# Kernel tuning notes

Measured on AMD Instinct MI355X. Metric: run time of the kernel, lower is better.

The kernel has to match this reference:

```python
import jax, jax.numpy as jnp
import numpy as np
from jax.scipy.special import gammaln, betaln

B, S, F, D, FEAT = 8, 128, 512, 256, 80


def conv1d(x, w, b, pad):
    # x: (B, C_in, L), w: (C_out, C_in, K) -> (B, C_out, L)
    y = jax.lax.conv_general_dilated(x, w, window_strides=(1,), padding=[(pad, pad)],
                                     dimension_numbers=('NCH', 'OIH', 'NCH'))
    return y + b[None, :, None]


def beta_binomial_log_prior(token_length, feat_length):
    # Vectorized betabinom(n=L-1, a=j+1, b=F_len-j).logpmf(k) over (B, S, F).
    k = jnp.arange(S, dtype=jnp.float32)[None, :, None]
    j = jnp.arange(F, dtype=jnp.float32)[None, None, :]
    L = token_length.astype(jnp.float32)[:, None, None]
    Fl = feat_length.astype(jnp.float32)[:, None, None]
    valid = (k < L) & (j < Fl)
    n = jnp.maximum(L - 1.0, 0.0)
    ks = jnp.minimum(k, n)                 # clamp outside-support k (masked anyway)
    a = j + 1.0                            # omega=1: a = i, i = j+1
    b = jnp.maximum(Fl - j, 1.0)           # b = F_len - i + 1 = F_len - j
    log_binom = gammaln(n + 1.0) - gammaln(ks + 1.0) - gammaln(n - ks + 1.0)
    lp = log_binom + betaln(ks + a, n - ks + b) - betaln(a, b)
    return jnp.where(valid, lp, -jnp.inf)


def setup_inputs() -> dict:
    key = jax.random.key(0)
    ks = jax.random.split(key, 10)
    h = jax.random.normal(ks[0], (B, S, D), jnp.float32)
    m = jax.random.normal(ks[1], (B, F, FEAT), jnp.float32)
    token_length = jax.random.randint(ks[2], (B,), S // 2, S + 1, dtype=jnp.int32)
    feat_length = jax.random.randint(ks[3], (B,), F // 2, F + 1, dtype=jnp.int32)
    mask = jnp.arange(S)[None, :] < token_length[:, None]
    w = lambda k, sh: jax.random.normal(k, sh, jnp.float32) * 0.02
    return dict(
        h=h, m=m,
        tw1=w(ks[4], (D, D, 3)), tb1=jnp.zeros((D,), jnp.float32),
        tw2=w(ks[5], (D, D, 1)), tb2=jnp.zeros((D,), jnp.float32),
        fw1=w(ks[6], (D, FEAT, 3)), fb1=jnp.zeros((D,), jnp.float32),
        fw2=w(ks[7], (D, D, 3)), fb2=jnp.zeros((D,), jnp.float32),
        fw3=w(ks[8], (D, D, 1)), fb3=jnp.zeros((D,), jnp.float32),
        mask=mask, token_length=token_length, feat_length=feat_length,
    )


def reference(h, m, tw1, tb1, tw2, tb2, fw1, fb1, fw2, fb2, fw3, fb3,
              mask, token_length, feat_length):
    # text conv stack: conv3(relu) -> conv1
    x = conv1d(h.transpose(0, 2, 1), tw1, tb1, 1)
    x = conv1d(jax.nn.relu(x), tw2, tb2, 0)
    hh = x.transpose(0, 2, 1)              # (B, S, D)
    # feat conv stack: conv3(relu) -> conv3(relu) -> conv1
    y = conv1d(m.transpose(0, 2, 1), fw1, fb1, 1)
    y = conv1d(jax.nn.relu(y), fw2, fb2, 1)
    y = conv1d(jax.nn.relu(y), fw3, fb3, 0)
    mm = y.transpose(0, 2, 1)              # (B, F, D)
    # broadcasted L2 pairwise distance -> (B, S, F)
    diff = hh[:, :, None, :] - mm[:, None, :, :]
    dist = jnp.sqrt(jnp.sum(diff * diff, axis=-1))
    logit = jnp.where(mask[:, :, None], -dist, -jnp.inf)
    log_a_soft = jax.nn.log_softmax(logit, axis=1)
    log_prior = beta_binomial_log_prior(token_length, feat_length)
    return log_prior + log_a_soft
```

## Files before the change

### kernel.cpp

```cpp
#include <hip/hip_runtime.h>
#include <cmath>

constexpr int B = 8, S = 128, F = 512, D = 256, FEAT = 80;
#define NEG_HUGE (-3.0e38f)

typedef unsigned short u16;
typedef unsigned int u32;
typedef __attribute__((ext_vector_type(8))) short bf16x8;
typedef __attribute__((ext_vector_type(4))) float f32x4;

#define MFMA(a, b, c) __builtin_amdgcn_mfma_f32_16x16x32_bf16((a), (b), (c), 0, 0, 0)

__device__ __forceinline__ u16 f2bf(float x) {
    u32 u = __float_as_uint(x);
    return (u16)((u + 0x7fffu + ((u >> 16) & 1u)) >> 16);
}
__device__ __forceinline__ float bf2f(u16 s) {
    return __uint_as_float(((u32)s) << 16);
}

constexpr int PRF = F + 2;
constexpr int PRH = S + 2;
constexpr int CIN_M = 96;

constexpr int N_G   = 1024;
constexpr int N_WT1 = 256 * 768;
constexpr int N_WT2 = 256 * 256;
constexpr int N_WF1 = 256 * 288;
constexpr int N_WF2 = 256 * 768;
constexpr int N_WF3 = 256 * 256;
constexpr int N_M   = B * PRF * CIN_M;
constexpr int N_H   = B * PRH * D;
constexpr int N_Y1P = B * 2 * D;
constexpr int PREP_TOTAL = N_G + N_WT1 + N_WT2 + N_WF1 + N_WF2 + N_WF3
                         + N_M + N_H + N_Y1P;

__device__ __forceinline__ void wconv_frag(const float* __restrict__ w,
                                           u16* __restrict__ o16,
                                           int I, int TAPS, int CINP, int idx) {
    int KSTEPS = TAPS * CINP / 32;
    int e    = idx & 7;
    int lane = (idx >> 3) & 63;
    int rest = idx >> 9;
    int kb   = rest % KSTEPS;
    int ct16 = rest / KSTEPS;
    int co = ct16 * 16 + (lane & 15);
    int k  = kb * 32 + (lane >> 4) * 8 + e;
    int tap = k / CINP, ci = k % CINP;
    float v = (ci < I) ? w[(co * I + ci) * TAPS + tap] : 0.f;
    o16[idx] = f2bf(v);
}

__global__ __launch_bounds__(256) void k_prep(
    const float* __restrict__ m, const float* __restrict__ h,
    const float* __restrict__ tw1, const float* __restrict__ tw2,
    const float* __restrict__ fw1, const float* __restrict__ fw2,
    const float* __restrict__ fw3,
    float* __restrict__ gt,
    u16* __restrict__ WT1, u16* __restrict__ WT2,
    u16* __restrict__ WF1, u16* __restrict__ WF2, u16* __restrict__ WF3,
    u16* __restrict__ M, u16* __restrict__ H, u16* __restrict__ Y1)
{
    int idx = blockIdx.x * 256 + threadIdx.x;
    if (idx < N_G) { gt[idx] = (float)lgamma((double)idx); return; }
    idx -= N_G;
    if (idx < N_WT1) { wconv_frag(tw1, WT1, 256, 3, 256, idx); return; }
    idx -= N_WT1;
    if (idx < N_WT2) { wconv_frag(tw2, WT2, 256, 1, 256, idx); return; }
    idx -= N_WT2;
    if (idx < N_WF1) { wconv_frag(fw1, WF1,  80, 3, CIN_M, idx); return; }
    idx -= N_WF1;
    if (idx < N_WF2) { wconv_frag(fw2, WF2, 256, 3, 256, idx); return; }
    idx -= N_WF2;
    if (idx < N_WF3) { wconv_frag(fw3, WF3, 256, 1, 256, idx); return; }
    idx -= N_WF3;
    if (idx < N_M) {
        int ci = idx % CIN_M;
        int p  = (idx / CIN_M) % PRF;
        int b  = idx / (CIN_M * PRF);
        float v = (p >= 1 && p <= F && ci < FEAT)
                ? m[(b * F + (p - 1)) * FEAT + ci] : 0.f;
        M[idx] = f2bf(v);
        return;
    }
    idx -= N_M;
    if (idx < N_H) {
        int ci = idx % D;
        int p  = (idx / D) % PRH;
        int b  = idx / (D * PRH);
        float v = (p >= 1 && p <= S) ? h[(b * S + (p - 1)) * D + ci] : 0.f;
        H[idx] = f2bf(v);
        return;
    }
    idx -= N_H;
    if (idx < N_Y1P) {
        int ci = idx % D;
        int which = (idx / D) & 1;
        int b = idx / (2 * D);
        int row = b * PRF + (which ? (PRF - 1) : 0);
        Y1[row * D + ci] = 0;
    }
}

constexpr int SHBYTES = 17408;

template<int CINP, int TAPS, bool RELU>
__device__ __forceinline__ void conv_block(
    char* shbuf,
    const u16* __restrict__ A, int arowbase,
    const u16* __restrict__ Wf, const float* __restrict__ bias, int co0,
    u16* __restrict__ O, int orowbase)
{
    constexpr int KTOT = TAPS * CINP;
    constexpr int KSTEPS = KTOT / 32;
    constexpr int KPT = CINP / 32;
    constexpr int ITER = (KSTEPS + 3) / 4;
    constexpr int ROWS = 32 + TAPS - 1;
    constexpr int RB = CINP * 2;

    const int t  = threadIdx.x;
    const int w  = t >> 6;
    const int l  = t & 63;
    const int lr = l & 15;
    const int kg = l >> 4;

    for (int c = t; c < ROWS * (CINP / 8); c += 256) {
        int row = c / (CINP / 8), cc = c % (CINP / 8);
        bf16x8 v = *(const bf16x8*)(A + (arowbase + row) * CINP + cc * 8);
        *(bf16x8*)(shbuf + row * RB + ((cc * 16) ^ ((row & 7) << 4))) = v;
    }
    __syncthreads();

    f32x4 a00 = {0.f, 0.f, 0.f, 0.f}, a01 = a00, a10 = a00, a11 = a00;
    const u16* wp0 = Wf + (size_t)(co0 >> 4) * KSTEPS * 512 + l * 8;
    const u16* wp1 = wp0 + (size_t)KSTEPS * 512;

#pragma unroll
    for (int i = 0; i < ITER; ++i) {
        int kb = w + 4 * i;
        if (KSTEPS % 4 == 0 || kb < KSTEPS) {
            int colb = (kb % KPT) * 64 + kg * 16;
            int rr0 = lr + kb / KPT;
            int rr1 = rr0 + 16;
            bf16x8 ah0 = *(const bf16x8*)(shbuf + rr0 * RB + (colb ^ ((rr0 & 7) << 4)));
            bf16x8 ah1 = *(const bf16x8*)(shbuf + rr1 * RB + (colb ^ ((rr1 & 7) << 4)));
            bf16x8 b0  = *(const bf16x8*)(wp0 + kb * 512);
            bf16x8 b1  = *(const bf16x8*)(wp1 + kb * 512);
            a00 = MFMA(ah0, b0, a00);
            a01 = MFMA(ah0, b1, a01);
            a10 = MFMA(ah1, b0, a10);
            a11 = MFMA(ah1, b1, a11);
        }
    }
    __syncthreads();

    float (*red)[64][17] = (float(*)[64][17])shbuf;
#pragma unroll
    for (int r = 0; r < 4; ++r) {
        red[w][l][0 * 4 + r] = a00[r];
        red[w][l][1 * 4 + r] = a01[r];
        red[w][l][2 * 4 + r] = a10[r];
        red[w][l][3 * 4 + r] = a11[r];
    }
    __syncthreads();

#pragma unroll
    for (int j = 0; j < 4; ++j) {
        int v = w * 4 + j;
        float s = red[0][l][v] + red[1][l][v] + red[2][l][v] + red[3][l][v];
        int m2 = v >> 3, ct = (v >> 2) & 1, r = v & 3;
        int co = co0 + ct * 16 + lr;
        int orow = orowbase + m2 * 16 + kg * 4 + r;
        float val = s + bias[co];
        if (RELU) val = fmaxf(val, 0.f);
        O[orow * 256 + co] = f2bf(val);
    }
}

__global__ __launch_bounds__(256) void k_convA(
    const u16* __restrict__ M, const u16* __restrict__ H,
    const u16* __restrict__ WF1, const u16* __restrict__ WT1,
    const float* __restrict__ fb1, const float* __restrict__ tb1,
    u16* __restrict__ Y1, u16* __restrict__ X1)
{
    __shared__ __align__(16) char shbuf[SHBYTES];
    int bid = blockIdx.x;
    if (bid < 1024) {
        int co0 = (bid & 7) * 32;
        int p0  = ((bid >> 3) & 15) * 32;
        int b   = bid >> 7;
        conv_block<CIN_M, 3, true>(shbuf, M, b * PRF + p0, WF1, fb1, co0,
                                   Y1, b * PRF + p0 + 1);
    } else {
        int i = bid - 1024;
        int co0 = (i & 7) * 32;
        int p0  = ((i >> 3) & 3) * 32;
        int b   = i >> 5;
        conv_block<D, 3, true>(shbuf, H, b * PRH + p0, WT1, tb1, co0,
                               X1, b * S + p0);
    }
}

__global__ __launch_bounds__(256) void k_convB(
    const u16* __restrict__ Y1, const u16* __restrict__ X1,
    const u16* __restrict__ WF2, const u16* __restrict__ WT2,
    const float* __restrict__ fb2, const float* __restrict__ tb2,
    u16* __restrict__ Y2, u16* __restrict__ Ho)
{
    __shared__ __align__(16) char shbuf[SHBYTES];
    int bid = blockIdx.x;
    if (bid < 1024) {
        int co0 = (bid & 7) * 32;
        int p0  = ((bid >> 3) & 15) * 32;
        int b   = bid >> 7;
        conv_block<D, 3, true>(shbuf, Y1, b * PRF + p0, WF2, fb2, co0,
                               Y2, b * F + p0);
    } else {
        int i = bid - 1024;
        int co0 = (i & 7) * 32;
        int p0  = ((i >> 3) & 3) * 32;
        int b   = i >> 5;
        conv_block<D, 1, false>(shbuf, X1, b * S + p0, WT2, tb2, co0,
                                Ho, b * S + p0);
    }
}

__global__ __launch_bounds__(512) void k_distsoft(
    const u16* __restrict__ Y2, const u16* __restrict__ Ho,
    const u16* __restrict__ WF3, const float* __restrict__ fb3,
    const float* __restrict__ gt,
    const int* __restrict__ tokl, const int* __restrict__ featl,
    float* __restrict__ out)
{
    __shared__ float gts[1024];
    __shared__ u16 mo[16 * 256];
    __shared__ float sc[128][18];
    __shared__ float red[512];
    __shared__ float na[128], nb[16], mcol[16], scol[16];
    int t = threadIdx.x;
    int b = blockIdx.x >> 5;
    int f0 = (blockIdx.x & 31) * 16;
    for (int i = t; i < 1024; i += 512) gts[i] = gt[i];
    int L = tokl[b], Fl = featl[b];

    int w = t >> 6, l = t & 63, lr = l & 15, kg = (l >> 4) & 3;

    {
        f32x4 acc0 = {0.f, 0.f, 0.f, 0.f}, acc1 = acc0;
        const u16* ap = Y2 + (b * F + f0 + lr) * 256 + kg * 8;
        const u16* wp = WF3 + (size_t)(2 * w) * 8 * 512 + l * 8;
#pragma unroll
        for (int kb = 0; kb < 8; ++kb) {
            bf16x8 av = *(const bf16x8*)(ap + kb * 32);
            bf16x8 b0 = *(const bf16x8*)(wp + kb * 512);
            bf16x8 b1 = *(const bf16x8*)(wp + (8 + kb) * 512);
            acc0 = MFMA(av, b0, acc0);
            acc1 = MFMA(av, b1, acc1);
        }
#pragma unroll
        for (int nt = 0; nt < 2; ++nt) {
            int co = w * 32 + nt * 16 + lr;
            float bv = fb3[co];
            const f32x4& a = nt == 0 ? acc0 : acc1;
#pragma unroll
            for (int r = 0; r < 4; ++r) {
                int pos = kg * 4 + r;
                int byte = pos * 512 + ((co * 2) ^ ((pos & 7) << 4));
                *(u16*)((char*)mo + byte) = f2bf(a[r] + bv);
            }
        }
    }
    __syncthreads();

    {
        int c = t >> 5;
        int byte = c * 512 + (((t & 31) * 16) ^ ((c & 7) << 4));
        bf16x8 v = *(const bf16x8*)((char*)mo + byte);
        float s = 0.f;
#pragma unroll
        for (int e = 0; e < 8; ++e) { float a = bf2f((u16)v[e]); s = fmaf(a, a, s); }
        red[t] = s;
    }
    __syncthreads();
    if (t < 16) {
        float s = 0.f;
#pragma unroll
        for (int j = 0; j < 32; ++j) s += red[t * 32 + j];
        nb[t] = s;
    }
    __syncthreads();

    {
        int r = t >> 2, kc = (t & 3) * 64;
        const u16* p = Ho + (b * S + r) * 256 + kc;
        float s = 0.f;
#pragma unroll
        for (int j = 0; j < 8; ++j) {
            bf16x8 v = *(const bf16x8*)(p + j * 8);
#pragma unroll
            for (int e = 0; e < 8; ++e) { float a = bf2f((u16)v[e]); s = fmaf(a, a, s); }
        }
        red[t] = s;
    }
    __syncthreads();
    if (t < 128) na[t] = red[4 * t] + red[4 * t + 1] + red[4 * t + 2] + red[4 * t + 3];

    f32x4 acc = {0.f, 0.f, 0.f, 0.f};
    {
        const u16* ap = Ho + (b * S + w * 16 + lr) * 256 + kg * 8;
        const char* bbase = (const char*)mo + lr * 512;
        int bx = (lr & 7) << 4;
#pragma unroll
        for (int kb = 0; kb < 8; ++kb) {
            bf16x8 a0 = *(const bf16x8*)(ap + kb * 32);
            bf16x8 bv = *(const bf16x8*)(bbase + ((kg * 16 + kb * 64) ^ bx));
            acc = MFMA(a0, bv, acc);
        }
    }
    __syncthreads();
#pragma unroll
    for (int r = 0; r < 4; ++r) {
        int sl = w * 16 + kg * 4 + r;
        float d2 = na[sl] + nb[lr] - 2.f * acc[r];
        sc[sl][lr] = -sqrtf(fmaxf(d2, 0.f));
    }
    __syncthreads();

    int fi = t & 15, sg = t >> 4;
    float sv[4], mx = -INFINITY;
#pragma unroll
    for (int i = 0; i < 4; ++i) {
        int s = sg + i * 32;
        float v = sc[s][fi];
        if (s >= L) v = -INFINITY;
        sv[i] = v;
        mx = fmaxf(mx, v);
    }
    red[t] = mx;
    __syncthreads();
    if (t < 16) {
        float m2 = -INFINITY;
#pragma unroll
        for (int j = 0; j < 32; ++j) m2 = fmaxf(m2, red[j * 16 + t]);
        mcol[t] = m2;
    }
    __syncthreads();
    float m = mcol[fi];
    float sum = 0.f;
#pragma unroll
    for (int i = 0; i < 4; ++i) sum += expf(sv[i] - m);
    red[t] = sum;
    __syncthreads();
    if (t < 16) {
        float s = 0.f;
#pragma unroll
        for (int j = 0; j < 32; ++j) s += red[j * 16 + t];
        scol[t] = s;
    }
    __syncthreads();
    float lse = m + logf(scol[fi]);

    int f = f0 + fi;
    float cb = gts[L] - gts[L + Fl] + gts[Fl + 1];
    bool fvalid = f < Fl;
    float cf = fvalid ? (-gts[f + 1] - gts[Fl - f]) : 0.f;
#pragma unroll
    for (int i = 0; i < 4; ++i) {
        int s = sg + i * 32;
        float o;
        if (s >= L || !fvalid) {
            o = NEG_HUGE;
        } else {
            float lp = cb + cf - gts[s + 1] - gts[L - s]
                     + gts[s + f + 1] + gts[L - 1 - s + Fl - f];
            o = lp + sv[i] - lse;
        }
        out[(b * S + s) * F + f] = o;
    }
}

extern "C" void kernel_launch(void* const* d_in, const int* in_sizes, int n_in,
                              void* d_out, int out_size, void* d_ws, size_t ws_size,
                              hipStream_t stream)
{
    const float* h   = (const float*)d_in[0];
    const float* m_  = (const float*)d_in[1];
    const float* tw1 = (const float*)d_in[2];
    const float* tb1 = (const float*)d_in[3];
    const float* tw2 = (const float*)d_in[4];
    const float* tb2 = (const float*)d_in[5];
    const float* fw1 = (const float*)d_in[6];
    const float* fb1 = (const float*)d_in[7];
    const float* fw2 = (const float*)d_in[8];
    const float* fb2 = (const float*)d_in[9];
    const float* fw3 = (const float*)d_in[10];
    const float* fb3 = (const float*)d_in[11];
    const int* tokl  = (const int*)d_in[13];
    const int* featl = (const int*)d_in[14];

    char* base = (char*)d_ws;
    size_t off = 0;
    auto alloc = [&](size_t bytes) -> char* {
        size_t a = (off + 255) & ~(size_t)255;
        off = a + bytes;
        return base + a;
    };

    float* gt = (float*)alloc(N_G * 4);
    u16* WT1 = (u16*)alloc(N_WT1 * 2);
    u16* WT2 = (u16*)alloc(N_WT2 * 2);
    u16* WF1 = (u16*)alloc(N_WF1 * 2);
    u16* WF2 = (u16*)alloc(N_WF2 * 2);
    u16* WF3 = (u16*)alloc(N_WF3 * 2);
    u16* M   = (u16*)alloc(N_M * 2);
    u16* H   = (u16*)alloc(N_H * 2);
    u16* Y1  = (u16*)alloc((size_t)B * PRF * D * 2);
    u16* Y2  = (u16*)alloc((size_t)B * F * D * 2);
    u16* X1  = (u16*)alloc((size_t)B * S * D * 2);
    u16* Ho  = (u16*)alloc((size_t)B * S * D * 2);
    float* out = (float*)d_out;

    k_prep<<<(PREP_TOTAL + 255) / 256, 256, 0, stream>>>(
        m_, h, tw1, tw2, fw1, fw2, fw3, gt,
        WT1, WT2, WF1, WF2, WF3, M, H, Y1);

    k_convA<<<1280, 256, 0, stream>>>(M, H, WF1, WT1, fb1, tb1, Y1, X1);
    k_convB<<<1280, 256, 0, stream>>>(Y1, X1, WF2, WT2, fb2, tb2, Y2, Ho);
    k_distsoft<<<B * (F / 16), 512, 0, stream>>>(Y2, Ho, WF3, fb3, gt,
                                                 tokl, featl, out);
}
```

Before: 35.67 us.

## Fuse input bf16 conversion into first conv and stage Ho in LDS

Drops the separate prep pass that converted and padded m and h into bf16 buffers; the first conv now reads fp32 inputs directly, converts them and zero-pads boundary rows while filling shared memory. The distance/softmax kernel copies the batch's Ho rows into a swizzled LDS tile once and uses it for both the norm and MFMA passes instead of reading global memory twice. This saves global traffic and prep work but adds a large LDS footprint per block and fp32 loads in the conv staging.

```diff
diff --git a/kernel.cpp b/kernel.cpp
--- a/kernel.cpp
+++ b/kernel.cpp
@@ -29,11 +29,8 @@
 constexpr int N_WF1 = 256 * 288;
 constexpr int N_WF2 = 256 * 768;
 constexpr int N_WF3 = 256 * 256;
-constexpr int N_M   = B * PRF * CIN_M;
-constexpr int N_H   = B * PRH * D;
 constexpr int N_Y1P = B * 2 * D;
-constexpr int PREP_TOTAL = N_G + N_WT1 + N_WT2 + N_WF1 + N_WF2 + N_WF3
-                         + N_M + N_H + N_Y1P;
+constexpr int PREP_TOTAL = N_G + N_WT1 + N_WT2 + N_WF1 + N_WF2 + N_WF3 + N_Y1P;
 
 __device__ __forceinline__ void wconv_frag(const float* __restrict__ w,
                                            u16* __restrict__ o16,
@@ -52,14 +49,13 @@
 }
 
 __global__ __launch_bounds__(256) void k_prep(
-    const float* __restrict__ m, const float* __restrict__ h,
     const float* __restrict__ tw1, const float* __restrict__ tw2,
     const float* __restrict__ fw1, const float* __restrict__ fw2,
     const float* __restrict__ fw3,
     float* __restrict__ gt,
     u16* __restrict__ WT1, u16* __restrict__ WT2,
     u16* __restrict__ WF1, u16* __restrict__ WF2, u16* __restrict__ WF3,
-    u16* __restrict__ M, u16* __restrict__ H, u16* __restrict__ Y1)
+    u16* __restrict__ Y1)
 {
     int idx = blockIdx.x * 256 + threadIdx.x;
     if (idx < N_G) { gt[idx] = (float)lgamma((double)idx); return; }
@@ -74,25 +70,6 @@
     idx -= N_WF2;
     if (idx < N_WF3) { wconv_frag(fw3, WF3, 256, 1, 256, idx); return; }
     idx -= N_WF3;
-    if (idx < N_M) {
-        int ci = idx % CIN_M;
-        int p  = (idx / CIN_M) % PRF;
-        int b  = idx / (CIN_M * PRF);
-        float v = (p >= 1 && p <= F && ci < FEAT)
-                ? m[(b * F + (p - 1)) * FEAT + ci] : 0.f;
-        M[idx] = f2bf(v);
-        return;
-    }
-    idx -= N_M;
-    if (idx < N_H) {
-        int ci = idx % D;
-        int p  = (idx / D) % PRH;
-        int b  = idx / (D * PRH);
-        float v = (p >= 1 && p <= S) ? h[(b * S + (p - 1)) * D + ci] : 0.f;
-        H[idx] = f2bf(v);
-        return;
-    }
-    idx -= N_H;
     if (idx < N_Y1P) {
         int ci = idx % D;
         int which = (idx / D) & 1;
@@ -104,10 +81,11 @@
 
 constexpr int SHBYTES = 17408;
 
-template<int CINP, int TAPS, bool RELU>
+template<int CINP, int TAPS, bool RELU, int MODE>
 __device__ __forceinline__ void conv_block(
     char* shbuf,
     const u16* __restrict__ A, int arowbase,
+    const float* __restrict__ src, int b, int p0,
     const u16* __restrict__ Wf, const float* __restrict__ bias, int co0,
     u16* __restrict__ O, int orowbase)
 {
@@ -117,6 +95,7 @@
     constexpr int ITER = (KSTEPS + 3) / 4;
     constexpr int ROWS = 32 + TAPS - 1;
     constexpr int RB = CINP * 2;
+    constexpr int G8 = CINP / 8;
 
     const int t  = threadIdx.x;
     const int w  = t >> 6;
@@ -124,9 +103,28 @@
     const int lr = l & 15;
     const int kg = l >> 4;
 
-    for (int c = t; c < ROWS * (CINP / 8); c += 256) {
-        int row = c / (CINP / 8), cc = c % (CINP / 8);
-        bf16x8 v = *(const bf16x8*)(A + (arowbase + row) * CINP + cc * 8);
+    for (int c = t; c < ROWS * G8; c += 256) {
+        int row = c / G8, cc = c % G8;
+        bf16x8 v;
+        if constexpr (MODE == 0) {
+            v = *(const bf16x8*)(A + (arowbase + row) * CINP + cc * 8);
+        } else {
+            constexpr int LIMIT = (MODE == 1) ? F : S;
+            constexpr int SSTR  = (MODE == 1) ? FEAT : D;
+            int pr = p0 + row;
+            bool valid = (pr >= 1) && (pr <= LIMIT) && (MODE == 2 || cc < FEAT / 8);
+            if (valid) {
+                const float* sp = src + ((size_t)(b * LIMIT + (pr - 1))) * SSTR + cc * 8;
+                float4 x0 = *(const float4*)sp;
+                float4 x1 = *(const float4*)(sp + 4);
+                v[0] = (short)f2bf(x0.x); v[1] = (short)f2bf(x0.y);
+                v[2] = (short)f2bf(x0.z); v[3] = (short)f2bf(x0.w);
+                v[4] = (short)f2bf(x1.x); v[5] = (short)f2bf(x1.y);
+                v[6] = (short)f2bf(x1.z); v[7] = (short)f2bf(x1.w);
+            } else {
+                v = bf16x8{0, 0, 0, 0, 0, 0, 0, 0};
+            }
+        }
         *(bf16x8*)(shbuf + row * RB + ((cc * 16) ^ ((row & 7) << 4))) = v;
     }
     __syncthreads();
@@ -178,7 +176,7 @@
 }
 
 __global__ __launch_bounds__(256) void k_convA(
-    const u16* __restrict__ M, const u16* __restrict__ H,
+    const float* __restrict__ m, const float* __restrict__ h,
     const u16* __restrict__ WF1, const u16* __restrict__ WT1,
     const float* __restrict__ fb1, const float* __restrict__ tb1,
     u16* __restrict__ Y1, u16* __restrict__ X1)
@@ -189,15 +187,15 @@
         int co0 = (bid & 7) * 32;
         int p0  = ((bid >> 3) & 15) * 32;
         int b   = bid >> 7;
-        conv_block<CIN_M, 3, true>(shbuf, M, b * PRF + p0, WF1, fb1, co0,
-                                   Y1, b * PRF + p0 + 1);
+        conv_block<CIN_M, 3, true, 1>(shbuf, nullptr, 0, m, b, p0,
+                                      WF1, fb1, co0, Y1, b * PRF + p0 + 1);
     } else {
         int i = bid - 1024;
         int co0 = (i & 7) * 32;
         int p0  = ((i >> 3) & 3) * 32;
         int b   = i >> 5;
-        conv_block<D, 3, true>(shbuf, H, b * PRH + p0, WT1, tb1, co0,
-                               X1, b * S + p0);
+        conv_block<D, 3, true, 2>(shbuf, nullptr, 0, h, b, p0,
+                                  WT1, tb1, co0, X1, b * S + p0);
     }
 }
 
@@ -213,15 +211,15 @@
         int co0 = (bid & 7) * 32;
         int p0  = ((bid >> 3) & 15) * 32;
         int b   = bid >> 7;
-        conv_block<D, 3, true>(shbuf, Y1, b * PRF + p0, WF2, fb2, co0,
-                               Y2, b * F + p0);
+        conv_block<D, 3, true, 0>(shbuf, Y1, b * PRF + p0, nullptr, 0, 0,
+                                  WF2, fb2, co0, Y2, b * F + p0);
     } else {
         int i = bid - 1024;
         int co0 = (i & 7) * 32;
         int p0  = ((i >> 3) & 3) * 32;
         int b   = i >> 5;
-        conv_block<D, 1, false>(shbuf, X1, b * S + p0, WT2, tb2, co0,
-                                Ho, b * S + p0);
+        conv_block<D, 1, false, 0>(shbuf, X1, b * S + p0, nullptr, 0, 0,
+                                   WT2, tb2, co0, Ho, b * S + p0);
     }
 }
 
@@ -233,6 +231,7 @@
     float* __restrict__ out)
 {
     __shared__ float gts[1024];
+    __shared__ __align__(16) u16 hol[128 * 256];
     __shared__ u16 mo[16 * 256];
     __shared__ float sc[128][18];
     __shared__ float red[512];
@@ -245,6 +244,12 @@
 
     int w = t >> 6, l = t & 63, lr = l & 15, kg = (l >> 4) & 3;
 
+    for (int c = t; c < 128 * 32; c += 512) {
+        int row = c >> 5, cc = c & 31;
+        bf16x8 v = *(const bf16x8*)(Ho + (b * S + row) * 256 + cc * 8);
+        *(bf16x8*)((char*)hol + row * 512 + ((cc * 16) ^ ((row & 7) << 4))) = v;
+    }
+
     {
         f32x4 acc0 = {0.f, 0.f, 0.f, 0.f}, acc1 = acc0;
         const u16* ap = Y2 + (b * F + f0 + lr) * 256 + kg * 8;
@@ -291,12 +296,13 @@
     __syncthreads();
 
     {
-        int r = t >> 2, kc = (t & 3) * 64;
-        const u16* p = Ho + (b * S + r) * 256 + kc;
+        int r = t >> 2;
+        int x = (r & 7) << 4;
         float s = 0.f;
 #pragma unroll
         for (int j = 0; j < 8; ++j) {
-            bf16x8 v = *(const bf16x8*)(p + j * 8);
+            int byte = r * 512 + ((((t & 3) * 128) + j * 16) ^ x);
+            bf16x8 v = *(const bf16x8*)((char*)hol + byte);
 #pragma unroll
             for (int e = 0; e < 8; ++e) { float a = bf2f((u16)v[e]); s = fmaf(a, a, s); }
         }
@@ -307,13 +313,16 @@
 
     f32x4 acc = {0.f, 0.f, 0.f, 0.f};
     {
-        const u16* ap = Ho + (b * S + w * 16 + lr) * 256 + kg * 8;
+        int rr = w * 16 + lr;
+        const char* abase = (const char*)hol + rr * 512;
+        int ax = (rr & 7) << 4;
         const char* bbase = (const char*)mo + lr * 512;
         int bx = (lr & 7) << 4;
 #pragma unroll
         for (int kb = 0; kb < 8; ++kb) {
-            bf16x8 a0 = *(const bf16x8*)(ap + kb * 32);
-            bf16x8 bv = *(const bf16x8*)(bbase + ((kg * 16 + kb * 64) ^ bx));
+            int colb = kg * 16 + kb * 64;
+            bf16x8 a0 = *(const bf16x8*)(abase + (colb ^ ax));
+            bf16x8 bv = *(const bf16x8*)(bbase + (colb ^ bx));
             acc = MFMA(a0, bv, acc);
         }
     }
@@ -412,8 +421,6 @@
     u16* WF1 = (u16*)alloc(N_WF1 * 2);
     u16* WF2 = (u16*)alloc(N_WF2 * 2);
     u16* WF3 = (u16*)alloc(N_WF3 * 2);
-    u16* M   = (u16*)alloc(N_M * 2);
-    u16* H   = (u16*)alloc(N_H * 2);
     u16* Y1  = (u16*)alloc((size_t)B * PRF * D * 2);
     u16* Y2  = (u16*)alloc((size_t)B * F * D * 2);
     u16* X1  = (u16*)alloc((size_t)B * S * D * 2);
@@ -421,10 +428,9 @@
     float* out = (float*)d_out;
 
     k_prep<<<(PREP_TOTAL + 255) / 256, 256, 0, stream>>>(
-        m_, h, tw1, tw2, fw1, fw2, fw3, gt,
-        WT1, WT2, WF1, WF2, WF3, M, H, Y1);
-
-    k_convA<<<1280, 256, 0, stream>>>(M, H, WF1, WT1, fb1, tb1, Y1, X1);
+        tw1, tw2, fw1, fw2, fw3, gt, WT1, WT2, WF1, WF2, WF3, Y1);
+
+    k_convA<<<1280, 256, 0, stream>>>(m_, h, WF1, WT1, fb1, tb1, Y1, X1);
     k_convB<<<1280, 256, 0, stream>>>(Y1, X1, WF2, WT2, fb2, tb2, Y2, Ho);
     k_distsoft<<<B * (F / 16), 512, 0, stream>>>(Y2, Ho, WF3, fb3, gt,
                                                  tokl, featl, out);
```

Measured after the change: 34.70 us (median of 3 runs). -2.7%, faster.
